# Kernel optimization log

Hardware: AMD Instinct MI355X
Metric: run time of the kernel (lower is better)

Reference implementation:

```python
import jax, jax.numpy as jnp
import numpy as np


def setup_inputs() -> dict:
    key = jax.random.key(0)
    ks = jax.random.split(key, 8)
    B, L, H, D = 128, 2048, 512, 512
    return {
        "batch": jax.random.normal(ks[0], (B, D), jnp.float32),
        "hid_states": jax.random.normal(ks[1], (B, L, H), jnp.float32),
        "h0": 0.1 * jax.random.normal(ks[2], (B, H), jnp.float32),
        "s0": 0.1 * jax.random.normal(ks[3], (B, H), jnp.float32),
        "W_ih": jax.random.normal(ks[4], (D, 4 * H), jnp.float32) * (1.0 / np.sqrt(D)),
        "W_hh": jax.random.normal(ks[5], (H, 4 * H), jnp.float32) * (1.0 / np.sqrt(H)),
        "b_lstm": jnp.zeros((4 * H,), jnp.float32),
        "W1": jax.random.normal(ks[6], (H, 64), jnp.float32) * (1.0 / np.sqrt(H)),
        "b1": jnp.zeros((64,), jnp.float32),
        "W2": jax.random.normal(ks[7], (64, D), jnp.float32) * (1.0 / np.sqrt(64)),
        "b2": jnp.zeros((D,), jnp.float32),
        "max_len": 10,
    }


def reference(batch, hid_states, h0, s0, W_ih, W_hh, b_lstm, W1, b1, W2, b2, max_len):
    B, D = batch.shape
    eps = 1e-8
    hs_sq = jnp.sum(hid_states * hid_states, axis=2)  # (B, L), loop-invariant

    def step(carry, _):
        x, h, s = carry
        # cosine-similarity attention of state s over recorded hidden states
        num = jnp.einsum('bh,blh->bl', s, hid_states)
        denom = jnp.sqrt(hs_sq * jnp.sum(s * s, axis=1, keepdims=True)) + eps
        energy = jax.nn.softmax(num / denom, axis=1)          # (B, L)
        context = jnp.einsum('blh,bl->bh', hid_states, energy)
        s = s + context
        # LSTM cell step (i, f, g, o gate order)
        gates = x @ W_ih + h @ W_hh + b_lstm
        i, f, g, o = jnp.split(gates, 4, axis=1)
        c = jax.nn.sigmoid(f) * s + jax.nn.sigmoid(i) * jnp.tanh(g)
        h = jax.nn.sigmoid(o) * jnp.tanh(c)
        # 2-layer MLP head produces next input
        x = jax.nn.leaky_relu(h @ W1 + b1, 0.01) @ W2 + b2
        return (x, h, c), x

    (_, _, _), outs = jax.lax.scan(step, (batch, h0, s0), None, length=max_len)
    # replicate torch: cat(dim=1) -> view(B, D, L) -> permute(0, 2, 1)
    flat = jnp.transpose(outs, (1, 0, 2)).reshape(B, max_len * D)
    return flat.reshape(B, D, max_len).transpose(0, 2, 1)
```

## Files before the change

### kernel.cpp

```cpp
#include <hip/hip_runtime.h>
#include <math.h>

#define B 128
#define L 2048
#define H 512
#define D 512
#define NG 2048
#define T 10
#define S 16
#define GB 256

#define OFF_S    ((size_t)0)
#define OFF_H    ((size_t)65536)
#define OFF_X    ((size_t)131072)
#define OFF_SS   ((size_t)196608)
#define OFF_G    ((size_t)196736)
#define OFF_PL   ((size_t)460928)
#define OFF_PCTX ((size_t)462976)
#define OFF_RN   ((size_t)1511552)
#define OFF_HB   ((size_t)1773696)

__device__ __forceinline__ float sigf(float x){ return 1.0f / (1.0f + __expf(-x)); }

__device__ __forceinline__ unsigned int b16r(float f){
    unsigned int u = __float_as_uint(f);
    return (u + 0x7FFFu + ((u >> 16) & 1u)) >> 16;
}
__device__ __forceinline__ unsigned int pack2(float lo, float hi){
    return b16r(lo) | (b16r(hi) << 16);
}

#define UNPK(u, f0, f1) { f0 = __uint_as_float((u) << 16); f1 = __uint_as_float((u) & 0xFFFF0000u); }

__device__ __forceinline__ float block_sum256(float v){
    for (int off = 32; off; off >>= 1) v += __shfl_xor(v, off, 64);
    __shared__ float r[4];
    int wave = threadIdx.x >> 6, lane = threadIdx.x & 63;
    if (lane == 0) r[wave] = v;
    __syncthreads();
    return r[0] + r[1] + r[2] + r[3];
}

__global__ void init_k(const float* __restrict__ s0, const float* __restrict__ h0,
                       const float* __restrict__ x0, float* __restrict__ ws){
    int b = blockIdx.x, t = threadIdx.x;
    float ssq = 0.f;
    for (int h = t; h < H; h += 256){
        float sv = s0[b*H + h];
        ws[OFF_S + b*H + h] = sv;
        ws[OFF_H + b*H + h] = h0[b*H + h];
        ssq += sv * sv;
    }
    for (int d = t; d < D; d += 256) ws[OFF_X + b*D + d] = x0[b*D + d];
    float tot = block_sum256(ssq);
    if (t == 0) ws[OFF_SS + b] = tot;
}

__device__ __forceinline__ void load_snorm(const float* __restrict__ ws, int b, int g, float* sf){
    const float* sb = ws + OFF_S + (size_t)b * H + g * 8;
    float rssb = rsqrtf(ws[OFF_SS + b]);
    #pragma unroll
    for (int cb = 0; cb < 4; cb++){
        float4 a = *(const float4*)(sb + cb*128);
        float4 c = *(const float4*)(sb + cb*128 + 4);
        sf[cb*8+0]=a.x*rssb; sf[cb*8+1]=a.y*rssb; sf[cb*8+2]=a.z*rssb; sf[cb*8+3]=a.w*rssb;
        sf[cb*8+4]=c.x*rssb; sf[cb*8+5]=c.y*rssb; sf[cb*8+6]=c.z*rssb; sf[cb*8+7]=c.w*rssb;
    }
}

__device__ __forceinline__ void attn_epilogue(float* ctx, float lsum, float* smem,
                                              float* __restrict__ ws, int b, int chunk,
                                              int wave, int g, int r){
    #pragma unroll
    for (int k = 0; k < 32; k++){
        ctx[k] += __shfl_xor(ctx[k], 16, 64);
        ctx[k] += __shfl_xor(ctx[k], 32, 64);
    }
    lsum += __shfl_xor(lsum, 16, 64);
    lsum += __shfl_xor(lsum, 32, 64);

    float (*lctx)[512] = (float(*)[512])smem;
    float* ll = smem + 2048;
    if (r == 0){
        #pragma unroll
        for (int cb = 0; cb < 4; cb++){
            float4 a = { ctx[cb*8+0], ctx[cb*8+1], ctx[cb*8+2], ctx[cb*8+3] };
            float4 c = { ctx[cb*8+4], ctx[cb*8+5], ctx[cb*8+6], ctx[cb*8+7] };
            *(float4*)&lctx[wave][cb*128 + g*8]     = a;
            *(float4*)&lctx[wave][cb*128 + g*8 + 4] = c;
        }
        if (g == 0) ll[wave] = lsum;
    }
    __syncthreads();
    int t = threadIdx.x;
    float* pc = ws + OFF_PCTX + ((size_t)b * S + chunk) * H;
    pc[t]       = lctx[0][t]     + lctx[1][t]     + lctx[2][t]     + lctx[3][t];
    pc[t + 256] = lctx[0][t+256] + lctx[1][t+256] + lctx[2][t+256] + lctx[3][t+256];
    if (t == 0) ws[OFF_PL + b*S + chunk] = ll[0] + ll[1] + ll[2] + ll[3];
}

__device__ __forceinline__ void attn_first_body(const float* __restrict__ hid,
                                                float* __restrict__ ws, int bid, float* smem){
    int b = bid >> 4, chunk = bid & (S - 1);
    int wave = threadIdx.x >> 6, lane = threadIdx.x & 63;
    int g = lane & 15, r = lane >> 4;
    float sf[32];
    load_snorm(ws, b, g, sf);

    int l0w = chunk * 128 + wave * 32;
    const float* hsrc = hid + ((size_t)b * L + l0w) * H + g * 8;
    uint4* hbdst = (uint4*)(ws + OFF_HB) + ((size_t)b * L + l0w) * 64 + g;
    float* rnw = ws + OFF_RN + (size_t)b * L + l0w;

    float ctx[32];
    #pragma unroll
    for (int k = 0; k < 32; k++) ctx[k] = 0.f;
    float lsum = 0.f;

    for (int it = 0; it < 8; it++){
        int ro = it*4 + r;
        const float* src = hsrc + (size_t)ro * H;
        float f[32];
        #pragma unroll
        for (int cb = 0; cb < 4; cb++){
            float4 a = *(const float4*)(src + cb*128);
            float4 c = *(const float4*)(src + cb*128 + 4);
            f[cb*8+0]=a.x; f[cb*8+1]=a.y; f[cb*8+2]=a.z; f[cb*8+3]=a.w;
            f[cb*8+4]=c.x; f[cb*8+5]=c.y; f[cb*8+6]=c.z; f[cb*8+7]=c.w;
        }
        float sq = 0.f, dot = 0.f;
        #pragma unroll
        for (int k = 0; k < 32; k++){ sq += f[k]*f[k]; dot += f[k]*sf[k]; }
        sq  += __shfl_xor(sq, 1, 64);  sq  += __shfl_xor(sq, 2, 64);
        sq  += __shfl_xor(sq, 4, 64);  sq  += __shfl_xor(sq, 8, 64);
        dot += __shfl_xor(dot, 1, 64); dot += __shfl_xor(dot, 2, 64);
        dot += __shfl_xor(dot, 4, 64); dot += __shfl_xor(dot, 8, 64);
        float rnv = rsqrtf(sq);
        if (g == 0) rnw[ro] = rnv;
        uint4* drow = hbdst + (size_t)ro * 64;
        #pragma unroll
        for (int cb = 0; cb < 4; cb++){
            uint4 o;
            o.x = pack2(f[cb*8+0], f[cb*8+1]);
            o.y = pack2(f[cb*8+2], f[cb*8+3]);
            o.z = pack2(f[cb*8+4], f[cb*8+5]);
            o.w = pack2(f[cb*8+6], f[cb*8+7]);
            drow[cb*16] = o;
        }
        float p = __expf(dot * rnv);
        lsum += p;
        #pragma unroll
        for (int k = 0; k < 32; k++) ctx[k] += p * f[k];
    }
    attn_epilogue(ctx, lsum, smem, ws, b, chunk, wave, g, r);
}

__device__ __forceinline__ void attn_steady_body(float* __restrict__ ws, int bid, float* smem){
    int b = bid >> 4, chunk = bid & (S - 1);
    int wave = threadIdx.x >> 6, lane = threadIdx.x & 63;
    int g = lane & 15, r = lane >> 4;
    float sf[32];
    load_snorm(ws, b, g, sf);

    int l0w = chunk * 128 + wave * 32;
    const uint4* hbu = (const uint4*)(ws + OFF_HB) + ((size_t)b * L + l0w) * 64 + g;
    const float* rnp = ws + OFF_RN + (size_t)b * L + l0w;

    float ctx[32];
    #pragma unroll
    for (int k = 0; k < 32; k++) ctx[k] = 0.f;
    float lsum = 0.f;

    for (int it = 0; it < 8; it++){
        int ro = it*4 + r;
        const uint4* hr = hbu + (size_t)ro * 64;
        uint4 u0 = hr[0];
        uint4 u1 = hr[16];
        uint4 u2 = hr[32];
        uint4 u3 = hr[48];
        float rnv = rnp[ro];
        float f[32];
        UNPK(u0.x, f[0], f[1])   UNPK(u0.y, f[2], f[3])
        UNPK(u0.z, f[4], f[5])   UNPK(u0.w, f[6], f[7])
        UNPK(u1.x, f[8], f[9])   UNPK(u1.y, f[10], f[11])
        UNPK(u1.z, f[12], f[13]) UNPK(u1.w, f[14], f[15])
        UNPK(u2.x, f[16], f[17]) UNPK(u2.y, f[18], f[19])
        UNPK(u2.z, f[20], f[21]) UNPK(u2.w, f[22], f[23])
        UNPK(u3.x, f[24], f[25]) UNPK(u3.y, f[26], f[27])
        UNPK(u3.z, f[28], f[29]) UNPK(u3.w, f[30], f[31])
        float dot = 0.f;
        #pragma unroll
        for (int k = 0; k < 32; k++) dot += f[k] * sf[k];
        dot += __shfl_xor(dot, 1, 64);
        dot += __shfl_xor(dot, 2, 64);
        dot += __shfl_xor(dot, 4, 64);
        dot += __shfl_xor(dot, 8, 64);
        float p = __expf(dot * rnv);
        lsum += p;
        #pragma unroll
        for (int k = 0; k < 32; k++) ctx[k] += p * f[k];
    }
    attn_epilogue(ctx, lsum, smem, ws, b, chunk, wave, g, r);
}

__device__ __forceinline__ void gates_body(const float* __restrict__ Wih,
                                           const float* __restrict__ Whh,
                                           const float* __restrict__ bias,
                                           float* __restrict__ ws,
                                           float* smem, int gid){
    int tid = threadIdx.x;
    int b0 = (gid >> 4) * 8, n0 = (gid & 15) * 128;
    float* xs  = smem;
    float* hsm = smem + 4096;
    {
        int r = tid >> 5, c = (tid & 31) * 16;
        const float* xsrc = ws + OFF_X + (size_t)(b0 + r) * D + c;
        const float* hsrc = ws + OFF_H + (size_t)(b0 + r) * H + c;
        #pragma unroll
        for (int j = 0; j < 4; j++){
            *(float4*)&xs[r*512 + c + j*4]  = *(const float4*)(xsrc + j*4);
            *(float4*)&hsm[r*512 + c + j*4] = *(const float4*)(hsrc + j*4);
        }
    }
    __syncthreads();
    int nt = tid & 31, kh = tid >> 5;
    int n = n0 + nt * 4;
    float4 acc[8];
    #pragma unroll
    for (int bi = 0; bi < 8; bi++){ acc[bi].x = 0.f; acc[bi].y = 0.f; acc[bi].z = 0.f; acc[bi].w = 0.f; }
    const float* w1p = Wih + (size_t)(kh * 64) * NG + n;
    const float* w2p = Whh + (size_t)(kh * 64) * NG + n;
    const float* xk = xs  + kh * 64;
    const float* hk = hsm + kh * 64;
    #pragma unroll 2
    for (int k = 0; k < 64; k++){
        float4 w1 = *(const float4*)(w1p + (size_t)k * NG);
        float4 w2 = *(const float4*)(w2p + (size_t)k * NG);
        #pragma unroll
        for (int bi = 0; bi < 8; bi++){
            float xv = xk[bi*512 + k], hv = hk[bi*512 + k];
            acc[bi].x += xv*w1.x + hv*w2.x;
            acc[bi].y += xv*w1.y + hv*w2.y;
            acc[bi].z += xv*w1.z + hv*w2.z;
            acc[bi].w += xv*w1.w + hv*w2.w;
        }
    }
    __syncthreads();
    float4* red = (float4*)smem;
    #pragma unroll
    for (int bi = 0; bi < 8; bi++) red[(kh*8 + bi)*32 + nt] = acc[bi];
    __syncthreads();
    int bi2 = tid >> 5, nt2 = tid & 31;
    int n2 = n0 + nt2 * 4;
    float4 s = *(const float4*)(bias + n2);
    #pragma unroll
    for (int k2 = 0; k2 < 8; k2++){
        float4 p = red[(k2*8 + bi2)*32 + nt2];
        s.x += p.x; s.y += p.y; s.z += p.z; s.w += p.w;
    }
    *(float4*)(ws + OFF_G + (size_t)(b0 + bi2)*NG + n2) = s;
}

__global__ __launch_bounds__(256, 3) void fused0_k(const float* __restrict__ hid,
                                                   const float* __restrict__ Wih,
                                                   const float* __restrict__ Whh,
                                                   const float* __restrict__ bias,
                                                   float* __restrict__ ws){
    __shared__ float smem[8192];
    if (blockIdx.x < GB){ gates_body(Wih, Whh, bias, ws, smem, blockIdx.x); return; }
    attn_first_body(hid, ws, blockIdx.x - GB, smem);
}

__global__ __launch_bounds__(256, 3) void fusedN_k(const float* __restrict__ Wih,
                                                   const float* __restrict__ Whh,
                                                   const float* __restrict__ bias,
                                                   float* __restrict__ ws){
    __shared__ float smem[8192];
    if (blockIdx.x < GB){ gates_body(Wih, Whh, bias, ws, smem, blockIdx.x); return; }
    attn_steady_body(ws, blockIdx.x - GB, smem);
}

__global__ __launch_bounds__(512) void tail_k(const float* __restrict__ W1, const float* __restrict__ b1,
                                              const float* __restrict__ W2, const float* __restrict__ b2,
                                              float* __restrict__ ws, float* __restrict__ out, int st){
    int b = blockIdx.x, t = threadIdx.x;
    __shared__ float hl[512];
    __shared__ float part[8][64];
    __shared__ float t1[64];
    __shared__ float rr[8];

    float Ls = 0.f;
    #pragma unroll
    for (int i = 0; i < S; i++) Ls += ws[OFF_PL + b*S + i];
    float inv = 1.0f / Ls;

    float cx = 0.f;
    #pragma unroll
    for (int i = 0; i < S; i++) cx += ws[OFF_PCTX + ((size_t)b*S + i)*H + t];
    const float* g = ws + OFF_G + (size_t)b * NG;
    float sn = ws[OFF_S + b*H + t] + cx * inv;
    float gi = g[t], gf = g[512 + t], gg = g[1024 + t], go = g[1536 + t];
    float c  = sigf(gf) * sn + sigf(gi) * tanhf(gg);
    float hv = sigf(go) * tanhf(c);
    ws[OFF_S + b*H + t] = c;
    ws[OFF_H + b*H + t] = hv;
    hl[t] = hv;
    float csq = c * c;
    for (int off = 32; off; off >>= 1) csq += __shfl_xor(csq, off, 64);
    int wv = t >> 6, ln = t & 63;
    if (ln == 0) rr[wv] = csq;
    __syncthreads();
    if (t == 0){
        float s = 0.f;
        #pragma unroll
        for (int i = 0; i < 8; i++) s += rr[i];
        ws[OFF_SS + b] = s;
    }

    int j = t & 63, q = t >> 6;
    float a = 0.f;
    #pragma unroll 4
    for (int k = q*64; k < q*64 + 64; k++) a += hl[k] * W1[k*64 + j];
    part[q][j] = a;
    __syncthreads();
    if (t < 64){
        float v = b1[t];
        #pragma unroll
        for (int i = 0; i < 8; i++) v += part[i][t];
        t1[t] = v > 0.f ? v : 0.01f * v;
    }
    __syncthreads();
    float a2 = b2[t];
    #pragma unroll
    for (int k = 0; k < 64; k++) a2 += t1[k] * W2[k*512 + t];
    ws[OFF_X + (size_t)b*D + t] = a2;
    int idx = st * D + t;
    out[(size_t)b * (D*T) + (size_t)(idx % T) * D + (idx / T)] = a2;
}

extern "C" void kernel_launch(void* const* d_in, const int* in_sizes, int n_in,
                              void* d_out, int out_size, void* d_ws, size_t ws_size,
                              hipStream_t stream) {
    const float* batch = (const float*)d_in[0];
    const float* hid   = (const float*)d_in[1];
    const float* h0    = (const float*)d_in[2];
    const float* s0    = (const float*)d_in[3];
    const float* Wih   = (const float*)d_in[4];
    const float* Whh   = (const float*)d_in[5];
    const float* bl    = (const float*)d_in[6];
    const float* W1    = (const float*)d_in[7];
    const float* b1    = (const float*)d_in[8];
    const float* W2    = (const float*)d_in[9];
    const float* b2    = (const float*)d_in[10];
    float* out = (float*)d_out;
    float* ws  = (float*)d_ws;

    init_k<<<B, 256, 0, stream>>>(s0, h0, batch, ws);
    fused0_k<<<B*S + GB, 256, 0, stream>>>(hid, Wih, Whh, bl, ws);
    tail_k<<<B, 512, 0, stream>>>(W1, b1, W2, b2, ws, out, 0);
    for (int st = 1; st < T; st++){
        fusedN_k<<<B*S + GB, 256, 0, stream>>>(Wih, Whh, bl, ws);
        tail_k<<<B, 512, 0, stream>>>(W1, b1, W2, b2, ws, out, st);
    }
}
```

Measured before the change: 1.419 ms.

## Fuse LSTM tail into step kernel via per-batch atomic ticket counters

Removes the separate tail kernel launch per step. Each attention or gates block bumps a per-batch atomic counter after its work, and the block that arrives last for a batch (32 contributors) runs the LSTM cell and MLP head inline. The init kernel no longer copies s0/h0/x0 into the workspace; step 0 reads the inputs directly. This cuts launch count and kernel-boundary gaps, at the cost of threadfences and atomics, plus serialized tail work on the finishing blocks (up to 8 batches for one gates block), done with 256 threads instead of 512.

After: 4.656 ms. 3.28x slower.

```diff
diff --git a/kernel.cpp b/kernel.cpp
--- a/kernel.cpp
+++ b/kernel.cpp
@@ -19,6 +19,7 @@
 #define OFF_PCTX ((size_t)462976)
 #define OFF_RN   ((size_t)1511552)
 #define OFF_HB   ((size_t)1773696)
+#define OFF_CNT  ((size_t)68882560)
 
 __device__ __forceinline__ float sigf(float x){ return 1.0f / (1.0f + __expf(-x)); }
 
@@ -41,24 +42,21 @@
     return r[0] + r[1] + r[2] + r[3];
 }
 
-__global__ void init_k(const float* __restrict__ s0, const float* __restrict__ h0,
-                       const float* __restrict__ x0, float* __restrict__ ws){
+__global__ void init_k(const float* __restrict__ s0, float* __restrict__ ws){
     int b = blockIdx.x, t = threadIdx.x;
     float ssq = 0.f;
     for (int h = t; h < H; h += 256){
         float sv = s0[b*H + h];
-        ws[OFF_S + b*H + h] = sv;
-        ws[OFF_H + b*H + h] = h0[b*H + h];
         ssq += sv * sv;
     }
-    for (int d = t; d < D; d += 256) ws[OFF_X + b*D + d] = x0[b*D + d];
     float tot = block_sum256(ssq);
     if (t == 0) ws[OFF_SS + b] = tot;
-}
-
-__device__ __forceinline__ void load_snorm(const float* __restrict__ ws, int b, int g, float* sf){
-    const float* sb = ws + OFF_S + (size_t)b * H + g * 8;
-    float rssb = rsqrtf(ws[OFF_SS + b]);
+    int* cnt = (int*)(ws + OFF_CNT);
+    for (int i = t; i < T; i += 256) cnt[i*B + b] = 0;
+}
+
+__device__ __forceinline__ void load_snorm(const float* __restrict__ sb_base, float rssb, int g, float* sf){
+    const float* sb = sb_base + g * 8;
     #pragma unroll
     for (int cb = 0; cb < 4; cb++){
         float4 a = *(const float4*)(sb + cb*128);
@@ -100,12 +98,13 @@
 }
 
 __device__ __forceinline__ void attn_first_body(const float* __restrict__ hid,
+                                                const float* __restrict__ sptr,
                                                 float* __restrict__ ws, int bid, float* smem){
     int b = bid >> 4, chunk = bid & (S - 1);
     int wave = threadIdx.x >> 6, lane = threadIdx.x & 63;
     int g = lane & 15, r = lane >> 4;
     float sf[32];
-    load_snorm(ws, b, g, sf);
+    load_snorm(sptr + (size_t)b * H, rsqrtf(ws[OFF_SS + b]), g, sf);
 
     int l0w = chunk * 128 + wave * 32;
     const float* hsrc = hid + ((size_t)b * L + l0w) * H + g * 8;
@@ -155,12 +154,13 @@
     attn_epilogue(ctx, lsum, smem, ws, b, chunk, wave, g, r);
 }
 
-__device__ __forceinline__ void attn_steady_body(float* __restrict__ ws, int bid, float* smem){
+__device__ __forceinline__ void attn_steady_body(const float* __restrict__ sptr,
+                                                 float* __restrict__ ws, int bid, float* smem){
     int b = bid >> 4, chunk = bid & (S - 1);
     int wave = threadIdx.x >> 6, lane = threadIdx.x & 63;
     int g = lane & 15, r = lane >> 4;
     float sf[32];
-    load_snorm(ws, b, g, sf);
+    load_snorm(sptr + (size_t)b * H, rsqrtf(ws[OFF_SS + b]), g, sf);
 
     int l0w = chunk * 128 + wave * 32;
     const uint4* hbu = (const uint4*)(ws + OFF_HB) + ((size_t)b * L + l0w) * 64 + g;
@@ -206,6 +206,8 @@
 __device__ __forceinline__ void gates_body(const float* __restrict__ Wih,
                                            const float* __restrict__ Whh,
                                            const float* __restrict__ bias,
+                                           const float* __restrict__ xp,
+                                           const float* __restrict__ hp,
                                            float* __restrict__ ws,
                                            float* smem, int gid){
     int tid = threadIdx.x;
@@ -214,8 +216,8 @@
     float* hsm = smem + 4096;
     {
         int r = tid >> 5, c = (tid & 31) * 16;
-        const float* xsrc = ws + OFF_X + (size_t)(b0 + r) * D + c;
-        const float* hsrc = ws + OFF_H + (size_t)(b0 + r) * H + c;
+        const float* xsrc = xp + (size_t)(b0 + r) * D + c;
+        const float* hsrc = hp + (size_t)(b0 + r) * H + c;
         #pragma unroll
         for (int j = 0; j < 4; j++){
             *(float4*)&xs[r*512 + c + j*4]  = *(const float4*)(xsrc + j*4);
@@ -261,81 +263,145 @@
     *(float4*)(ws + OFF_G + (size_t)(b0 + bi2)*NG + n2) = s;
 }
 
-__global__ __launch_bounds__(256, 3) void fused0_k(const float* __restrict__ hid,
-                                                   const float* __restrict__ Wih,
-                                                   const float* __restrict__ Whh,
-                                                   const float* __restrict__ bias,
-                                                   float* __restrict__ ws){
-    __shared__ float smem[8192];
-    if (blockIdx.x < GB){ gates_body(Wih, Whh, bias, ws, smem, blockIdx.x); return; }
-    attn_first_body(hid, ws, blockIdx.x - GB, smem);
-}
-
-__global__ __launch_bounds__(256, 3) void fusedN_k(const float* __restrict__ Wih,
-                                                   const float* __restrict__ Whh,
-                                                   const float* __restrict__ bias,
-                                                   float* __restrict__ ws){
-    __shared__ float smem[8192];
-    if (blockIdx.x < GB){ gates_body(Wih, Whh, bias, ws, smem, blockIdx.x); return; }
-    attn_steady_body(ws, blockIdx.x - GB, smem);
-}
-
-__global__ __launch_bounds__(512) void tail_k(const float* __restrict__ W1, const float* __restrict__ b1,
-                                              const float* __restrict__ W2, const float* __restrict__ b2,
-                                              float* __restrict__ ws, float* __restrict__ out, int st){
-    int b = blockIdx.x, t = threadIdx.x;
-    __shared__ float hl[512];
-    __shared__ float part[8][64];
-    __shared__ float t1[64];
-    __shared__ float rr[8];
+__device__ __forceinline__ void tail_body(const float* __restrict__ W1, const float* __restrict__ b1,
+                                          const float* __restrict__ W2, const float* __restrict__ b2,
+                                          const float* __restrict__ sread,
+                                          float* __restrict__ ws, float* __restrict__ out,
+                                          int st, int b, float* smem){
+    int t = threadIdx.x;
+    float* hl  = smem;
+    float* prt = smem + 512;
+    float* t1  = smem + 768;
+    float* rr  = smem + 832;
+    __syncthreads();
 
     float Ls = 0.f;
     #pragma unroll
     for (int i = 0; i < S; i++) Ls += ws[OFF_PL + b*S + i];
     float inv = 1.0f / Ls;
 
-    float cx = 0.f;
-    #pragma unroll
-    for (int i = 0; i < S; i++) cx += ws[OFF_PCTX + ((size_t)b*S + i)*H + t];
     const float* g = ws + OFF_G + (size_t)b * NG;
-    float sn = ws[OFF_S + b*H + t] + cx * inv;
-    float gi = g[t], gf = g[512 + t], gg = g[1024 + t], go = g[1536 + t];
-    float c  = sigf(gf) * sn + sigf(gi) * tanhf(gg);
-    float hv = sigf(go) * tanhf(c);
-    ws[OFF_S + b*H + t] = c;
-    ws[OFF_H + b*H + t] = hv;
-    hl[t] = hv;
-    float csq = c * c;
+    float csq = 0.f;
+    #pragma unroll
+    for (int half = 0; half < 2; half++){
+        int idx = half*256 + t;
+        float cx = 0.f;
+        #pragma unroll
+        for (int i = 0; i < S; i++) cx += ws[OFF_PCTX + ((size_t)b*S + i)*H + idx];
+        float sn = sread[(size_t)b*H + idx] + cx * inv;
+        float gi = g[idx], gf = g[512 + idx], gg = g[1024 + idx], go = g[1536 + idx];
+        float c  = sigf(gf) * sn + sigf(gi) * tanhf(gg);
+        float hv = sigf(go) * tanhf(c);
+        ws[OFF_S + (size_t)b*H + idx] = c;
+        ws[OFF_H + (size_t)b*H + idx] = hv;
+        hl[idx] = hv;
+        csq += c * c;
+    }
     for (int off = 32; off; off >>= 1) csq += __shfl_xor(csq, off, 64);
     int wv = t >> 6, ln = t & 63;
     if (ln == 0) rr[wv] = csq;
     __syncthreads();
-    if (t == 0){
-        float s = 0.f;
-        #pragma unroll
-        for (int i = 0; i < 8; i++) s += rr[i];
-        ws[OFF_SS + b] = s;
-    }
+    if (t == 0) ws[OFF_SS + b] = rr[0] + rr[1] + rr[2] + rr[3];
 
     int j = t & 63, q = t >> 6;
     float a = 0.f;
     #pragma unroll 4
-    for (int k = q*64; k < q*64 + 64; k++) a += hl[k] * W1[k*64 + j];
-    part[q][j] = a;
+    for (int k = q*128; k < q*128 + 128; k++) a += hl[k] * W1[k*64 + j];
+    prt[q*64 + j] = a;
     __syncthreads();
     if (t < 64){
-        float v = b1[t];
-        #pragma unroll
-        for (int i = 0; i < 8; i++) v += part[i][t];
+        float v = b1[t] + prt[t] + prt[64 + t] + prt[128 + t] + prt[192 + t];
         t1[t] = v > 0.f ? v : 0.01f * v;
     }
     __syncthreads();
-    float a2 = b2[t];
-    #pragma unroll
-    for (int k = 0; k < 64; k++) a2 += t1[k] * W2[k*512 + t];
-    ws[OFF_X + (size_t)b*D + t] = a2;
-    int idx = st * D + t;
-    out[(size_t)b * (D*T) + (size_t)(idx % T) * D + (idx / T)] = a2;
+    #pragma unroll
+    for (int half = 0; half < 2; half++){
+        int d = half*256 + t;
+        float a2 = b2[d];
+        #pragma unroll 8
+        for (int k = 0; k < 64; k++) a2 += t1[k] * W2[k*512 + d];
+        ws[OFF_X + (size_t)b*D + d] = a2;
+        int idx = st * D + d;
+        out[(size_t)b * (D*T) + (size_t)(idx % T) * D + (idx / T)] = a2;
+    }
+    __syncthreads();
+}
+
+__device__ __forceinline__ void ticket_and_tail(const float* __restrict__ W1, const float* __restrict__ b1,
+                                                const float* __restrict__ W2, const float* __restrict__ b2,
+                                                const float* __restrict__ sread,
+                                                float* __restrict__ ws, float* __restrict__ out,
+                                                int st, int myb, int b0g, float* smem,
+                                                int* nfin_sh, int* finb_sh){
+    __syncthreads();
+    __threadfence();
+    __syncthreads();
+    if (threadIdx.x == 0){
+        int* cnt = (int*)(ws + OFF_CNT) + st * B;
+        int nf = 0;
+        if (b0g >= 0){
+            #pragma unroll
+            for (int i = 0; i < 8; i++){
+                int old = atomicAdd(&cnt[b0g + i], 1);
+                if (old == 31) finb_sh[nf++] = b0g + i;
+            }
+        } else {
+            int old = atomicAdd(&cnt[myb], 1);
+            if (old == 31) finb_sh[nf++] = myb;
+        }
+        *nfin_sh = nf;
+    }
+    __syncthreads();
+    int nf = *nfin_sh;
+    if (nf > 0){
+        __threadfence();
+        for (int i = 0; i < nf; i++)
+            tail_body(W1, b1, W2, b2, sread, ws, out, st, finb_sh[i], smem);
+    }
+}
+
+__global__ __launch_bounds__(256, 3) void step0_k(const float* __restrict__ hid,
+                                                  const float* __restrict__ batch,
+                                                  const float* __restrict__ h0,
+                                                  const float* __restrict__ s0,
+                                                  const float* __restrict__ Wih,
+                                                  const float* __restrict__ Whh,
+                                                  const float* __restrict__ bias,
+                                                  const float* __restrict__ W1, const float* __restrict__ b1,
+                                                  const float* __restrict__ W2, const float* __restrict__ b2,
+                                                  float* __restrict__ ws, float* __restrict__ out){
+    __shared__ float smem[8192];
+    __shared__ int nfin; __shared__ int finb[8];
+    int myb = -1, b0g = -1;
+    if (blockIdx.x < GB){
+        b0g = ((int)blockIdx.x >> 4) * 8;
+        gates_body(Wih, Whh, bias, batch, h0, ws, smem, blockIdx.x);
+    } else {
+        int bid = blockIdx.x - GB;
+        myb = bid >> 4;
+        attn_first_body(hid, s0, ws, bid, smem);
+    }
+    ticket_and_tail(W1, b1, W2, b2, s0, ws, out, 0, myb, b0g, smem, &nfin, finb);
+}
+
+__global__ __launch_bounds__(256, 3) void stepN_k(const float* __restrict__ Wih,
+                                                  const float* __restrict__ Whh,
+                                                  const float* __restrict__ bias,
+                                                  const float* __restrict__ W1, const float* __restrict__ b1,
+                                                  const float* __restrict__ W2, const float* __restrict__ b2,
+                                                  float* __restrict__ ws, float* __restrict__ out, int st){
+    __shared__ float smem[8192];
+    __shared__ int nfin; __shared__ int finb[8];
+    int myb = -1, b0g = -1;
+    if (blockIdx.x < GB){
+        b0g = ((int)blockIdx.x >> 4) * 8;
+        gates_body(Wih, Whh, bias, ws + OFF_X, ws + OFF_H, ws, smem, blockIdx.x);
+    } else {
+        int bid = blockIdx.x - GB;
+        myb = bid >> 4;
+        attn_steady_body(ws + OFF_S, ws, bid, smem);
+    }
+    ticket_and_tail(W1, b1, W2, b2, ws + OFF_S, ws, out, st, myb, b0g, smem, &nfin, finb);
 }
 
 extern "C" void kernel_launch(void* const* d_in, const int* in_sizes, int n_in,
@@ -355,11 +421,8 @@
     float* out = (float*)d_out;
     float* ws  = (float*)d_ws;
 
-    init_k<<<B, 256, 0, stream>>>(s0, h0, batch, ws);
-    fused0_k<<<B*S + GB, 256, 0, stream>>>(hid, Wih, Whh, bl, ws);
-    tail_k<<<B, 512, 0, stream>>>(W1, b1, W2, b2, ws, out, 0);
-    for (int st = 1; st < T; st++){
-        fusedN_k<<<B*S + GB, 256, 0, stream>>>(Wih, Whh, bl, ws);
-        tail_k<<<B, 512, 0, stream>>>(W1, b1, W2, b2, ws, out, st);
-    }
-}
+    init_k<<<B, 256, 0, stream>>>(s0, ws);
+    step0_k<<<B*S + GB, 256, 0, stream>>>(hid, batch, h0, s0, Wih, Whh, bl, W1, b1, W2, b2, ws, out);
+    for (int st = 1; st < T; st++)
+        stepN_k<<<B*S + GB, 256, 0, stream>>>(Wih, Whh, bl, W1, b1, W2, b2, ws, out, st);
+}
```

## Fuse LSTM cell tail into next step kernel with double-buffered workspace

Applied to the files above, without the earlier changes.

Removes the separate init and tail kernels by having each step kernel recompute the previous step's cell update: gate blocks rebuild h and the MLP output x for their batch rows, and attention blocks rebuild the new state s and its norm. Workspace buffers are double-buffered by step parity so the reads and writes of consecutive steps do not conflict, and a final kernel finishes the last step. This cuts the kernel launches and inter-kernel gaps roughly in half. In exchange the cell and MLP math is computed redundantly across many blocks, and the partial-context reductions are read more often.

New measurement: 1.640 ms. +15.6%, slower.

```diff
diff --git a/kernel.cpp b/kernel.cpp
--- a/kernel.cpp
+++ b/kernel.cpp
@@ -10,15 +10,12 @@
 #define S 16
 #define GB 256
 
-#define OFF_S    ((size_t)0)
-#define OFF_H    ((size_t)65536)
-#define OFF_X    ((size_t)131072)
-#define OFF_SS   ((size_t)196608)
-#define OFF_G    ((size_t)196736)
-#define OFF_PL   ((size_t)460928)
-#define OFF_PCTX ((size_t)462976)
-#define OFF_RN   ((size_t)1511552)
-#define OFF_HB   ((size_t)1773696)
+#define OFF_SB(p)   ((size_t)(p)*65536)
+#define OFF_G(p)    ((size_t)131072 + (size_t)(p)*262144)
+#define OFF_PL(p)   ((size_t)655360 + (size_t)(p)*2048)
+#define OFF_PCTX(p) ((size_t)659456 + (size_t)(p)*1048576)
+#define OFF_RN      ((size_t)2756608)
+#define OFF_HB      ((size_t)3018752)
 
 __device__ __forceinline__ float sigf(float x){ return 1.0f / (1.0f + __expf(-x)); }
 
@@ -32,33 +29,16 @@
 
 #define UNPK(u, f0, f1) { f0 = __uint_as_float((u) << 16); f1 = __uint_as_float((u) & 0xFFFF0000u); }
 
-__device__ __forceinline__ float block_sum256(float v){
+__device__ __forceinline__ float block_sum256(float v, float* r4){
     for (int off = 32; off; off >>= 1) v += __shfl_xor(v, off, 64);
-    __shared__ float r[4];
     int wave = threadIdx.x >> 6, lane = threadIdx.x & 63;
-    if (lane == 0) r[wave] = v;
+    if (lane == 0) r4[wave] = v;
     __syncthreads();
-    return r[0] + r[1] + r[2] + r[3];
-}
-
-__global__ void init_k(const float* __restrict__ s0, const float* __restrict__ h0,
-                       const float* __restrict__ x0, float* __restrict__ ws){
-    int b = blockIdx.x, t = threadIdx.x;
-    float ssq = 0.f;
-    for (int h = t; h < H; h += 256){
-        float sv = s0[b*H + h];
-        ws[OFF_S + b*H + h] = sv;
-        ws[OFF_H + b*H + h] = h0[b*H + h];
-        ssq += sv * sv;
-    }
-    for (int d = t; d < D; d += 256) ws[OFF_X + b*D + d] = x0[b*D + d];
-    float tot = block_sum256(ssq);
-    if (t == 0) ws[OFF_SS + b] = tot;
-}
-
-__device__ __forceinline__ void load_snorm(const float* __restrict__ ws, int b, int g, float* sf){
-    const float* sb = ws + OFF_S + (size_t)b * H + g * 8;
-    float rssb = rsqrtf(ws[OFF_SS + b]);
+    return r4[0] + r4[1] + r4[2] + r4[3];
+}
+
+__device__ __forceinline__ void load_snorm(const float* sptr, float rssb, int g, float* sf){
+    const float* sb = sptr + g * 8;
     #pragma unroll
     for (int cb = 0; cb < 4; cb++){
         float4 a = *(const float4*)(sb + cb*128);
@@ -69,7 +49,7 @@
 }
 
 __device__ __forceinline__ void attn_epilogue(float* ctx, float lsum, float* smem,
-                                              float* __restrict__ ws, int b, int chunk,
+                                              float* __restrict__ pl, float* __restrict__ pc,
                                               int wave, int g, int r){
     #pragma unroll
     for (int k = 0; k < 32; k++){
@@ -79,8 +59,8 @@
     lsum += __shfl_xor(lsum, 16, 64);
     lsum += __shfl_xor(lsum, 32, 64);
 
-    float (*lctx)[512] = (float(*)[512])smem;
-    float* ll = smem + 2048;
+    float (*lctx)[512] = (float(*)[512])(smem + 520);
+    float* ll = smem + 520 + 2048;
     if (r == 0){
         #pragma unroll
         for (int cb = 0; cb < 4; cb++){
@@ -93,19 +73,20 @@
     }
     __syncthreads();
     int t = threadIdx.x;
-    float* pc = ws + OFF_PCTX + ((size_t)b * S + chunk) * H;
     pc[t]       = lctx[0][t]     + lctx[1][t]     + lctx[2][t]     + lctx[3][t];
     pc[t + 256] = lctx[0][t+256] + lctx[1][t+256] + lctx[2][t+256] + lctx[3][t+256];
-    if (t == 0) ws[OFF_PL + b*S + chunk] = ll[0] + ll[1] + ll[2] + ll[3];
-}
-
-__device__ __forceinline__ void attn_first_body(const float* __restrict__ hid,
-                                                float* __restrict__ ws, int bid, float* smem){
-    int b = bid >> 4, chunk = bid & (S - 1);
+    if (t == 0) pl[0] = ll[0] + ll[1] + ll[2] + ll[3];
+}
+
+__device__ __forceinline__ void attn_main_first(const float* __restrict__ hid,
+                                                const float* sptr, float rssb,
+                                                float* __restrict__ ws, float* smem,
+                                                float* __restrict__ pl, float* __restrict__ pc,
+                                                int b, int chunk){
     int wave = threadIdx.x >> 6, lane = threadIdx.x & 63;
     int g = lane & 15, r = lane >> 4;
     float sf[32];
-    load_snorm(ws, b, g, sf);
+    load_snorm(sptr, rssb, g, sf);
 
     int l0w = chunk * 128 + wave * 32;
     const float* hsrc = hid + ((size_t)b * L + l0w) * H + g * 8;
@@ -152,15 +133,17 @@
         #pragma unroll
         for (int k = 0; k < 32; k++) ctx[k] += p * f[k];
     }
-    attn_epilogue(ctx, lsum, smem, ws, b, chunk, wave, g, r);
-}
-
-__device__ __forceinline__ void attn_steady_body(float* __restrict__ ws, int bid, float* smem){
-    int b = bid >> 4, chunk = bid & (S - 1);
+    attn_epilogue(ctx, lsum, smem, pl, pc, wave, g, r);
+}
+
+__device__ __forceinline__ void attn_main_steady(const float* sptr, float rssb,
+                                                 const float* __restrict__ ws, float* smem,
+                                                 float* __restrict__ pl, float* __restrict__ pc,
+                                                 int b, int chunk){
     int wave = threadIdx.x >> 6, lane = threadIdx.x & 63;
     int g = lane & 15, r = lane >> 4;
     float sf[32];
-    load_snorm(ws, b, g, sf);
+    load_snorm(sptr, rssb, g, sf);
 
     int l0w = chunk * 128 + wave * 32;
     const uint4* hbu = (const uint4*)(ws + OFF_HB) + ((size_t)b * L + l0w) * 64 + g;
@@ -200,142 +183,226 @@
         #pragma unroll
         for (int k = 0; k < 32; k++) ctx[k] += p * f[k];
     }
-    attn_epilogue(ctx, lsum, smem, ws, b, chunk, wave, g, r);
-}
-
-__device__ __forceinline__ void gates_body(const float* __restrict__ Wih,
-                                           const float* __restrict__ Whh,
-                                           const float* __restrict__ bias,
-                                           float* __restrict__ ws,
-                                           float* smem, int gid){
+    attn_epilogue(ctx, lsum, smem, pl, pc, wave, g, r);
+}
+
+__global__ __launch_bounds__(256, 3) void step_k(const float* __restrict__ hid,
+                                                 const float* __restrict__ batch,
+                                                 const float* __restrict__ h0,
+                                                 const float* __restrict__ s0,
+                                                 const float* __restrict__ Wih,
+                                                 const float* __restrict__ Whh,
+                                                 const float* __restrict__ bias,
+                                                 const float* __restrict__ W1, const float* __restrict__ b1,
+                                                 const float* __restrict__ W2, const float* __restrict__ b2,
+                                                 float* __restrict__ ws, float* __restrict__ out, int st){
+    __shared__ float smem[8704];
+    const int par = st & 1, q = par ^ 1;
     int tid = threadIdx.x;
-    int b0 = (gid >> 4) * 8, n0 = (gid & 15) * 128;
-    float* xs  = smem;
-    float* hsm = smem + 4096;
-    {
-        int r = tid >> 5, c = (tid & 31) * 16;
-        const float* xsrc = ws + OFF_X + (size_t)(b0 + r) * D + c;
-        const float* hsrc = ws + OFF_H + (size_t)(b0 + r) * H + c;
-        #pragma unroll
-        for (int j = 0; j < 4; j++){
-            *(float4*)&xs[r*512 + c + j*4]  = *(const float4*)(xsrc + j*4);
-            *(float4*)&hsm[r*512 + c + j*4] = *(const float4*)(hsrc + j*4);
-        }
+
+    if (blockIdx.x < GB){
+        int gid = blockIdx.x;
+        int b0 = (gid >> 4) * 8, ntile = gid & 15, n0 = ntile * 128;
+        float* xs  = smem;
+        float* hsm = smem + 4096;
+        float* t1s = smem + 8192;
+
+        if (st == 0){
+            int r = tid >> 5, c = (tid & 31) * 16;
+            #pragma unroll
+            for (int j = 0; j < 4; j++){
+                *(float4*)&xs[r*512 + c + j*4]  = *(const float4*)(batch + (size_t)(b0 + r)*D + c + j*4);
+                *(float4*)&hsm[r*512 + c + j*4] = *(const float4*)(h0 + (size_t)(b0 + r)*H + c + j*4);
+            }
+        } else {
+            int bi = tid >> 5, u = tid & 31;
+            int b = b0 + bi;
+            const float* plq = ws + OFF_PL(q) + b*S;
+            float Ls = 0.f;
+            #pragma unroll
+            for (int i = 0; i < S; i++) Ls += plq[i];
+            float inv = 1.0f / Ls;
+            float cx[16];
+            #pragma unroll
+            for (int e = 0; e < 16; e++) cx[e] = 0.f;
+            #pragma unroll 2
+            for (int i = 0; i < S; i++){
+                const float* p = ws + OFF_PCTX(q) + ((size_t)(b*S + i))*H + u*16;
+                #pragma unroll
+                for (int e4 = 0; e4 < 4; e4++){
+                    float4 v = *(const float4*)(p + e4*4);
+                    cx[e4*4+0] += v.x; cx[e4*4+1] += v.y; cx[e4*4+2] += v.z; cx[e4*4+3] += v.w;
+                }
+            }
+            const float* gg = ws + OFF_G(q) + (size_t)b * NG;
+            const float* sprev = (st == 1 ? s0 : ws + OFF_SB(q)) + (size_t)b * H;
+            #pragma unroll
+            for (int e = 0; e < 16; e++){
+                int idx = u*16 + e;
+                float sn = sprev[idx] + cx[e]*inv;
+                float c  = sigf(gg[512 + idx]) * sn + sigf(gg[idx]) * tanhf(gg[1024 + idx]);
+                hsm[bi*512 + idx] = sigf(gg[1536 + idx]) * tanhf(c);
+            }
+            __syncthreads();
+            float a0 = 0.f, a1 = 0.f;
+            for (int k = 0; k < 512; k++){
+                float hv = hsm[bi*512 + k];
+                a0 += hv * W1[k*64 + u];
+                a1 += hv * W1[k*64 + u + 32];
+            }
+            a0 += b1[u]; a1 += b1[u + 32];
+            t1s[bi*64 + u]      = a0 > 0.f ? a0 : 0.01f*a0;
+            t1s[bi*64 + u + 32] = a1 > 0.f ? a1 : 0.01f*a1;
+            __syncthreads();
+            float xacc[16];
+            #pragma unroll
+            for (int e = 0; e < 16; e++) xacc[e] = b2[u*16 + e];
+            for (int k = 0; k < 64; k++){
+                float tv = t1s[bi*64 + k];
+                const float* wp = W2 + (size_t)k*512 + u*16;
+                #pragma unroll
+                for (int e4 = 0; e4 < 4; e4++){
+                    float4 wv = *(const float4*)(wp + e4*4);
+                    xacc[e4*4+0] += tv*wv.x; xacc[e4*4+1] += tv*wv.y;
+                    xacc[e4*4+2] += tv*wv.z; xacc[e4*4+3] += tv*wv.w;
+                }
+            }
+            #pragma unroll
+            for (int e = 0; e < 16; e++) xs[bi*512 + u*16 + e] = xacc[e];
+            if (ntile == 0){
+                #pragma unroll
+                for (int e = 0; e < 16; e++){
+                    int d = u*16 + e;
+                    int idx = (st - 1)*D + d;
+                    out[(size_t)b*(D*T) + (size_t)(idx % T)*D + (idx / T)] = xacc[e];
+                }
+            }
+        }
+        __syncthreads();
+        int nt = tid & 31, kh = tid >> 5;
+        int n = n0 + nt * 4;
+        float4 acc[8];
+        #pragma unroll
+        for (int bi = 0; bi < 8; bi++){ acc[bi].x = 0.f; acc[bi].y = 0.f; acc[bi].z = 0.f; acc[bi].w = 0.f; }
+        const float* w1p = Wih + (size_t)(kh * 64) * NG + n;
+        const float* w2p = Whh + (size_t)(kh * 64) * NG + n;
+        const float* xk = xs  + kh * 64;
+        const float* hk = hsm + kh * 64;
+        #pragma unroll 2
+        for (int k = 0; k < 64; k++){
+            float4 w1 = *(const float4*)(w1p + (size_t)k * NG);
+            float4 w2 = *(const float4*)(w2p + (size_t)k * NG);
+            #pragma unroll
+            for (int bi = 0; bi < 8; bi++){
+                float xv = xk[bi*512 + k], hv = hk[bi*512 + k];
+                acc[bi].x += xv*w1.x + hv*w2.x;
+                acc[bi].y += xv*w1.y + hv*w2.y;
+                acc[bi].z += xv*w1.z + hv*w2.z;
+                acc[bi].w += xv*w1.w + hv*w2.w;
+            }
+        }
+        __syncthreads();
+        float4* red = (float4*)smem;
+        #pragma unroll
+        for (int bi = 0; bi < 8; bi++) red[(kh*8 + bi)*32 + nt] = acc[bi];
+        __syncthreads();
+        int bi2 = tid >> 5, nt2 = tid & 31;
+        int n2 = n0 + nt2 * 4;
+        float4 sg = *(const float4*)(bias + n2);
+        #pragma unroll
+        for (int k2 = 0; k2 < 8; k2++){
+            float4 p = red[(k2*8 + bi2)*32 + nt2];
+            sg.x += p.x; sg.y += p.y; sg.z += p.z; sg.w += p.w;
+        }
+        *(float4*)(ws + OFF_G(par) + (size_t)(b0 + bi2)*NG + n2) = sg;
+    } else {
+        int bid = blockIdx.x - GB;
+        int b = bid >> 4, chunk = bid & (S - 1);
+        float* pl = ws + OFF_PL(par) + b*S + chunk;
+        float* pc = ws + OFF_PCTX(par) + ((size_t)(b*S + chunk))*H;
+
+        if (st == 0){
+            float ssq = 0.f;
+            #pragma unroll
+            for (int hh = 0; hh < 2; hh++){
+                float sv = s0[(size_t)b*H + hh*256 + tid];
+                ssq += sv * sv;
+            }
+            float rssb = rsqrtf(block_sum256(ssq, smem + 8448));
+            attn_main_first(hid, s0 + (size_t)b*H, rssb, ws, smem, pl, pc, b, chunk);
+        } else {
+            float* sc = smem;
+            const float* plq = ws + OFF_PL(q) + b*S;
+            float Ls = 0.f;
+            #pragma unroll
+            for (int i = 0; i < S; i++) Ls += plq[i];
+            float inv = 1.0f / Ls;
+            const float* gg = ws + OFF_G(q) + (size_t)b * NG;
+            const float* sprev = (st == 1 ? s0 : ws + OFF_SB(q)) + (size_t)b * H;
+            float ssq = 0.f;
+            #pragma unroll
+            for (int hh = 0; hh < 2; hh++){
+                int idx = hh*256 + tid;
+                float cxv = 0.f;
+                #pragma unroll
+                for (int i = 0; i < S; i++) cxv += ws[OFF_PCTX(q) + ((size_t)(b*S + i))*H + idx];
+                float sn = sprev[idx] + cxv*inv;
+                float c  = sigf(gg[512 + idx]) * sn + sigf(gg[idx]) * tanhf(gg[1024 + idx]);
+                sc[idx] = c;
+                ssq += c * c;
+                if (chunk == 0) ws[OFF_SB(par) + (size_t)b*H + idx] = c;
+            }
+            float rssb = rsqrtf(block_sum256(ssq, smem + 8448));
+            attn_main_steady(sc, rssb, ws, smem, pl, pc, b, chunk);
+        }
+    }
+}
+
+__global__ __launch_bounds__(256) void final_k(const float* __restrict__ W1, const float* __restrict__ b1,
+                                               const float* __restrict__ W2, const float* __restrict__ b2,
+                                               float* __restrict__ ws, float* __restrict__ out){
+    int b = blockIdx.x, tid = threadIdx.x;
+    __shared__ float hl[512];
+    __shared__ float prt[256];
+    __shared__ float t1[64];
+    const float* plq = ws + OFF_PL(1) + b*S;
+    float Ls = 0.f;
+    #pragma unroll
+    for (int i = 0; i < S; i++) Ls += plq[i];
+    float inv = 1.0f / Ls;
+    const float* gg = ws + OFF_G(1) + (size_t)b * NG;
+    const float* sprev = ws + OFF_SB(1) + (size_t)b * H;
+    #pragma unroll
+    for (int hh = 0; hh < 2; hh++){
+        int idx = hh*256 + tid;
+        float cxv = 0.f;
+        #pragma unroll
+        for (int i = 0; i < S; i++) cxv += ws[OFF_PCTX(1) + ((size_t)(b*S + i))*H + idx];
+        float sn = sprev[idx] + cxv*inv;
+        float c  = sigf(gg[512 + idx]) * sn + sigf(gg[idx]) * tanhf(gg[1024 + idx]);
+        hl[idx] = sigf(gg[1536 + idx]) * tanhf(c);
     }
     __syncthreads();
-    int nt = tid & 31, kh = tid >> 5;
-    int n = n0 + nt * 4;
-    float4 acc[8];
-    #pragma unroll
-    for (int bi = 0; bi < 8; bi++){ acc[bi].x = 0.f; acc[bi].y = 0.f; acc[bi].z = 0.f; acc[bi].w = 0.f; }
-    const float* w1p = Wih + (size_t)(kh * 64) * NG + n;
-    const float* w2p = Whh + (size_t)(kh * 64) * NG + n;
-    const float* xk = xs  + kh * 64;
-    const float* hk = hsm + kh * 64;
-    #pragma unroll 2
-    for (int k = 0; k < 64; k++){
-        float4 w1 = *(const float4*)(w1p + (size_t)k * NG);
-        float4 w2 = *(const float4*)(w2p + (size_t)k * NG);
-        #pragma unroll
-        for (int bi = 0; bi < 8; bi++){
-            float xv = xk[bi*512 + k], hv = hk[bi*512 + k];
-            acc[bi].x += xv*w1.x + hv*w2.x;
-            acc[bi].y += xv*w1.y + hv*w2.y;
-            acc[bi].z += xv*w1.z + hv*w2.z;
-            acc[bi].w += xv*w1.w + hv*w2.w;
-        }
-    }
-    __syncthreads();
-    float4* red = (float4*)smem;
-    #pragma unroll
-    for (int bi = 0; bi < 8; bi++) red[(kh*8 + bi)*32 + nt] = acc[bi];
-    __syncthreads();
-    int bi2 = tid >> 5, nt2 = tid & 31;
-    int n2 = n0 + nt2 * 4;
-    float4 s = *(const float4*)(bias + n2);
-    #pragma unroll
-    for (int k2 = 0; k2 < 8; k2++){
-        float4 p = red[(k2*8 + bi2)*32 + nt2];
-        s.x += p.x; s.y += p.y; s.z += p.z; s.w += p.w;
-    }
-    *(float4*)(ws + OFF_G + (size_t)(b0 + bi2)*NG + n2) = s;
-}
-
-__global__ __launch_bounds__(256, 3) void fused0_k(const float* __restrict__ hid,
-                                                   const float* __restrict__ Wih,
-                                                   const float* __restrict__ Whh,
-                                                   const float* __restrict__ bias,
-                                                   float* __restrict__ ws){
-    __shared__ float smem[8192];
-    if (blockIdx.x < GB){ gates_body(Wih, Whh, bias, ws, smem, blockIdx.x); return; }
-    attn_first_body(hid, ws, blockIdx.x - GB, smem);
-}
-
-__global__ __launch_bounds__(256, 3) void fusedN_k(const float* __restrict__ Wih,
-                                                   const float* __restrict__ Whh,
-                                                   const float* __restrict__ bias,
-                                                   float* __restrict__ ws){
-    __shared__ float smem[8192];
-    if (blockIdx.x < GB){ gates_body(Wih, Whh, bias, ws, smem, blockIdx.x); return; }
-    attn_steady_body(ws, blockIdx.x - GB, smem);
-}
-
-__global__ __launch_bounds__(512) void tail_k(const float* __restrict__ W1, const float* __restrict__ b1,
-                                              const float* __restrict__ W2, const float* __restrict__ b2,
-                                              float* __restrict__ ws, float* __restrict__ out, int st){
-    int b = blockIdx.x, t = threadIdx.x;
-    __shared__ float hl[512];
-    __shared__ float part[8][64];
-    __shared__ float t1[64];
-    __shared__ float rr[8];
-
-    float Ls = 0.f;
-    #pragma unroll
-    for (int i = 0; i < S; i++) Ls += ws[OFF_PL + b*S + i];
-    float inv = 1.0f / Ls;
-
-    float cx = 0.f;
-    #pragma unroll
-    for (int i = 0; i < S; i++) cx += ws[OFF_PCTX + ((size_t)b*S + i)*H + t];
-    const float* g = ws + OFF_G + (size_t)b * NG;
-    float sn = ws[OFF_S + b*H + t] + cx * inv;
-    float gi = g[t], gf = g[512 + t], gg = g[1024 + t], go = g[1536 + t];
-    float c  = sigf(gf) * sn + sigf(gi) * tanhf(gg);
-    float hv = sigf(go) * tanhf(c);
-    ws[OFF_S + b*H + t] = c;
-    ws[OFF_H + b*H + t] = hv;
-    hl[t] = hv;
-    float csq = c * c;
-    for (int off = 32; off; off >>= 1) csq += __shfl_xor(csq, off, 64);
-    int wv = t >> 6, ln = t & 63;
-    if (ln == 0) rr[wv] = csq;
-    __syncthreads();
-    if (t == 0){
-        float s = 0.f;
-        #pragma unroll
-        for (int i = 0; i < 8; i++) s += rr[i];
-        ws[OFF_SS + b] = s;
-    }
-
-    int j = t & 63, q = t >> 6;
+    int j = tid & 63, q4 = tid >> 6;
     float a = 0.f;
     #pragma unroll 4
-    for (int k = q*64; k < q*64 + 64; k++) a += hl[k] * W1[k*64 + j];
-    part[q][j] = a;
+    for (int k = q4*128; k < q4*128 + 128; k++) a += hl[k] * W1[k*64 + j];
+    prt[q4*64 + j] = a;
     __syncthreads();
-    if (t < 64){
-        float v = b1[t];
-        #pragma unroll
-        for (int i = 0; i < 8; i++) v += part[i][t];
-        t1[t] = v > 0.f ? v : 0.01f * v;
+    if (tid < 64){
+        float v = b1[tid] + prt[tid] + prt[64 + tid] + prt[128 + tid] + prt[192 + tid];
+        t1[tid] = v > 0.f ? v : 0.01f*v;
     }
     __syncthreads();
-    float a2 = b2[t];
-    #pragma unroll
-    for (int k = 0; k < 64; k++) a2 += t1[k] * W2[k*512 + t];
-    ws[OFF_X + (size_t)b*D + t] = a2;
-    int idx = st * D + t;
-    out[(size_t)b * (D*T) + (size_t)(idx % T) * D + (idx / T)] = a2;
+    #pragma unroll
+    for (int hh = 0; hh < 2; hh++){
+        int d = hh*256 + tid;
+        float a2 = b2[d];
+        #pragma unroll 8
+        for (int k = 0; k < 64; k++) a2 += t1[k] * W2[k*512 + d];
+        int idx = 9*D + d;
+        out[(size_t)b*(D*T) + (size_t)(idx % T)*D + (idx / T)] = a2;
+    }
 }
 
 extern "C" void kernel_launch(void* const* d_in, const int* in_sizes, int n_in,
@@ -355,11 +422,8 @@
     float* out = (float*)d_out;
     float* ws  = (float*)d_ws;
 
-    init_k<<<B, 256, 0, stream>>>(s0, h0, batch, ws);
-    fused0_k<<<B*S + GB, 256, 0, stream>>>(hid, Wih, Whh, bl, ws);
-    tail_k<<<B, 512, 0, stream>>>(W1, b1, W2, b2, ws, out, 0);
-    for (int st = 1; st < T; st++){
-        fusedN_k<<<B*S + GB, 256, 0, stream>>>(Wih, Whh, bl, ws);
-        tail_k<<<B, 512, 0, stream>>>(W1, b1, W2, b2, ws, out, st);
-    }
-}
+    for (int st = 0; st < T; st++)
+        step_k<<<B*S + GB, 256, 0, stream>>>(hid, batch, h0, s0, Wih, Whh, bl,
+                                             W1, b1, W2, b2, ws, out, st);
+    final_k<<<B, 256, 0, stream>>>(W1, b1, W2, b2, ws, out);
+}
```
